# Kernel tuning notes

Measured on AMD Instinct MI355X. Metric: run time of the kernel, lower is better.

Reference implementation:

```python
import jax, jax.numpy as jnp
import numpy as np

N = 50000       # nodes
E = 800000      # directed edges (before self-loops)
F_IN = 256      # input node features
HID = 64        # hidden_channels
HEADS = 4       # heads of conv1
NEG_SLOPE = 0.2 # PyG GATConv LeakyReLU slope


def setup_inputs() -> dict:
    key = jax.random.key(0)
    ks = jax.random.split(key, 10)
    x = jax.random.normal(ks[0], (N, F_IN), dtype=jnp.float32)
    edge_index = jax.random.randint(ks[1], (2, E), 0, N, dtype=jnp.int32)
    # GATConv params: lin weight [F_in, H*C], att_src/att_dst [H, C], bias
    W1 = jax.random.normal(ks[2], (F_IN, HEADS * HID), jnp.float32) * (1.0 / np.sqrt(F_IN))
    att_src1 = jax.random.normal(ks[3], (HEADS, HID), jnp.float32) * (1.0 / np.sqrt(HID))
    att_dst1 = jax.random.normal(ks[4], (HEADS, HID), jnp.float32) * (1.0 / np.sqrt(HID))
    b1 = jnp.zeros((HEADS * HID,), jnp.float32)
    W2 = jax.random.normal(ks[5], (HEADS * HID, HID), jnp.float32) * (1.0 / np.sqrt(HEADS * HID))
    att_src2 = jax.random.normal(ks[6], (1, HID), jnp.float32) * (1.0 / np.sqrt(HID))
    att_dst2 = jax.random.normal(ks[7], (1, HID), jnp.float32) * (1.0 / np.sqrt(HID))
    b2 = jnp.zeros((HID,), jnp.float32)
    return dict(x=x, edge_index=edge_index, W1=W1, att_src1=att_src1,
                att_dst1=att_dst1, b1=b1, W2=W2, att_src2=att_src2,
                att_dst2=att_dst2, b2=b2)


def gat_layer(x, src, dst, W, a_src, a_dst, bias, heads, ch, concat):
    n = x.shape[0]
    xh = (x @ W).reshape(n, heads, ch)                      # [N,H,C]
    al_s = jnp.einsum('nhc,hc->nh', xh, a_src)              # [N,H]
    al_d = jnp.einsum('nhc,hc->nh', xh, a_dst)
    e = jax.nn.leaky_relu(al_s[src] + al_d[dst], NEG_SLOPE) # [Etot,H]
    # segment softmax over incoming edges of each dst node
    m = jax.ops.segment_max(e, dst, num_segments=n)         # every node has a self-loop
    ex = jnp.exp(e - m[dst])
    den = jax.ops.segment_sum(ex, dst, num_segments=n)
    alpha = ex / (den[dst] + 1e-16)                         # [Etot,H]
    out = jax.ops.segment_sum(alpha[:, :, None] * xh[src], dst, num_segments=n)  # [N,H,C]
    out = out.reshape(n, heads * ch) if concat else out.mean(axis=1)
    return out + bias


def reference(x, edge_index, W1, att_src1, att_dst1, b1, W2, att_src2, att_dst2, b2):
    # GATConv default add_self_loops=True
    loops = jnp.arange(x.shape[0], dtype=edge_index.dtype)
    src = jnp.concatenate([edge_index[0], loops])
    dst = jnp.concatenate([edge_index[1], loops])
    h = jax.nn.elu(gat_layer(x, src, dst, W1, att_src1, att_dst1, b1, HEADS, HID, True))
    # dropout omitted (eval mode)
    out = jax.nn.elu(gat_layer(h, src, dst, W2, att_src2, att_dst2, b2, 1, HID, False))
    return out
```

## Files before the change

kernel.cpp:

```cpp
#include <hip/hip_runtime.h>
#include <math.h>


using short8_t  = __attribute__((ext_vector_type(8))) short;
using f32x4     = __attribute__((ext_vector_type(4))) float;
using ushort4v  = __attribute__((ext_vector_type(4))) unsigned short;
using ushort8v  = __attribute__((ext_vector_type(8))) unsigned short;
using half4     = __attribute__((ext_vector_type(4))) _Float16;

__device__ __forceinline__ float leaky02(float t) { return t > 0.f ? t : 0.2f * t; }
__device__ __forceinline__ float elu1(float t) { return t > 0.f ? t : (__expf(t) - 1.f); }

__device__ __forceinline__ unsigned short bf16_rne(float f) {
  unsigned u = __float_as_uint(f);
  unsigned r = u + 0x7FFFu + ((u >> 16) & 1u);
  return (unsigned short)(r >> 16);
}
__device__ __forceinline__ float bf16_to_f(unsigned short h) {
  return __uint_as_float(((unsigned)h) << 16);
}


__global__ __launch_bounds__(256) void count_kernel(const int* __restrict__ dst,
                                                    int* __restrict__ count, int E) {
  int e = blockIdx.x * blockDim.x + threadIdx.x;
  if (e < E) atomicAdd(&count[dst[e]], 1);
}

__global__ __launch_bounds__(256) void scan1_kernel(const int* __restrict__ count,
                                                    int* __restrict__ locpre,
                                                    int* __restrict__ bsum, int n) {
  __shared__ int sh[256];
  int t = threadIdx.x;
  int node = blockIdx.x * 256 + t;
  int v = (node < n) ? (1 + count[node]) : 0;
  sh[t] = v;
  __syncthreads();
  for (int off = 1; off < 256; off <<= 1) {
    int u = (t >= off) ? sh[t - off] : 0;
    __syncthreads();
    sh[t] += u;
    __syncthreads();
  }
  if (node < n) locpre[node] = sh[t] - v;
  if (t == 255) bsum[blockIdx.x] = sh[255];
}

__global__ __launch_bounds__(256) void scan2_kernel(int* __restrict__ bsum, int nb) {
  __shared__ int sh[256];
  int t = threadIdx.x;
  int v = (t < nb) ? bsum[t] : 0;
  sh[t] = v;
  __syncthreads();
  for (int off = 1; off < 256; off <<= 1) {
    int u = (t >= off) ? sh[t - off] : 0;
    __syncthreads();
    sh[t] += u;
    __syncthreads();
  }
  if (t < nb) bsum[t] = sh[t] - v;
}

__global__ __launch_bounds__(256) void scan3_kernel(const int* __restrict__ locpre,
                                                    const int* __restrict__ bsum,
                                                    int* __restrict__ offsets,
                                                    int* __restrict__ csr,
                                                    int* __restrict__ cursor,
                                                    int n, int Etot) {
  int node = blockIdx.x * 256 + threadIdx.x;
  if (node >= n) return;
  int o = bsum[blockIdx.x] + locpre[node];
  offsets[node] = o;
  csr[o] = node;
  cursor[node] = 0;
  if (node == n - 1) offsets[n] = Etot;
}

__global__ __launch_bounds__(256) void scatter_kernel(const int* __restrict__ src,
                                                      const int* __restrict__ dst,
                                                      const int* __restrict__ offsets,
                                                      int* __restrict__ cursor,
                                                      int* __restrict__ csr, int E) {
  int e = blockIdx.x * blockDim.x + threadIdx.x;
  if (e < E) {
    int d = dst[e];
    int pos = atomicAdd(&cursor[d], 1);
    csr[offsets[d] + 1 + pos] = src[e];
  }
}

__global__ __launch_bounds__(256) void convB_kernel(const float* __restrict__ W,
                                                    unsigned short* __restrict__ Bth,
                                                    unsigned short* __restrict__ Btl, int N) {
  int idx = blockIdx.x * blockDim.x + threadIdx.x;
  if (idx >= N * 64) return;
  int n = idx >> 6;
  int k4 = (idx & 63) * 4;
  ushort4v hi, lo;
#pragma unroll
  for (int i = 0; i < 4; ++i) {
    float w = W[(size_t)(k4 + i) * N + n];
    hi[i] = bf16_rne(w);
    lo[i] = bf16_rne(w - bf16_to_f(hi[i]));
  }
  size_t base = (size_t)n * 256 + k4;
  *(ushort4v*)&Bth[base] = hi;
  *(ushort4v*)&Btl[base] = lo;
}

template <int BN, int WR, int WC, int H, bool AF32>
__global__ __launch_bounds__(256) void gemm_fused(
    const float* __restrict__ Af,
    const unsigned short* __restrict__ Ah, const unsigned short* __restrict__ Al,
    const unsigned short* __restrict__ Bh, const unsigned short* __restrict__ Bl,
    const float* __restrict__ asrc, const float* __restrict__ adst,
    _Float16* __restrict__ xh, float* __restrict__ als, float* __restrict__ ald,
    int M, int N) {
  constexpr int BM = 128, BK = 32, KTOT = 256;
  constexpr int WM = BM / WR, WN = BN / WC;
  constexpr int MR = WM / 16, NR = WN / 16;
  constexpr int BROUNDS = (BN * 4) / 256;
  __shared__ __align__(16) unsigned short lsAh[BM * BK];
  __shared__ __align__(16) unsigned short lsAl[BM * BK];
  __shared__ __align__(16) unsigned short lsBh[BN * BK];
  __shared__ __align__(16) unsigned short lsBl[BN * BK];
  const int tid = threadIdx.x;
  const int lane = tid & 63;
  const int w = tid >> 6;
  const int wr = w / WC, wc = w % WC;
  const int bm = blockIdx.x * BM;
  const int bn = blockIdx.y * BN;

  f32x4 acc[MR][NR];
#pragma unroll
  for (int i = 0; i < MR; ++i)
#pragma unroll
    for (int j = 0; j < NR; ++j) acc[i][j] = (f32x4){0.f, 0.f, 0.f, 0.f};

  for (int k0 = 0; k0 < KTOT; k0 += BK) {
#pragma unroll
    for (int rnd = 0; rnd < 2; ++rnd) {
      int id = rnd * 256 + tid;
      int row = id >> 2, c0 = id & 3;
      int cs = c0 ^ ((row >> 1) & 3);
      bool ok = (bm + row) < M;
      ushort8v hi, lo;
      if (AF32) {
        float vv[8];
        if (ok) {
          float4 v0 = *(const float4*)&Af[(size_t)(bm + row) * 256 + k0 + c0 * 8];
          float4 v1 = *(const float4*)&Af[(size_t)(bm + row) * 256 + k0 + c0 * 8 + 4];
          vv[0] = v0.x; vv[1] = v0.y; vv[2] = v0.z; vv[3] = v0.w;
          vv[4] = v1.x; vv[5] = v1.y; vv[6] = v1.z; vv[7] = v1.w;
        } else {
#pragma unroll
          for (int i = 0; i < 8; ++i) vv[i] = 0.f;
        }
#pragma unroll
        for (int i = 0; i < 8; ++i) {
          hi[i] = bf16_rne(vv[i]);
          lo[i] = bf16_rne(vv[i] - bf16_to_f(hi[i]));
        }
      } else {
        if (ok) {
          hi = *(const ushort8v*)&Ah[(size_t)(bm + row) * 256 + k0 + c0 * 8];
          lo = *(const ushort8v*)&Al[(size_t)(bm + row) * 256 + k0 + c0 * 8];
        } else {
#pragma unroll
          for (int i = 0; i < 8; ++i) { hi[i] = 0; lo[i] = 0; }
        }
      }
      *(ushort8v*)&lsAh[row * BK + cs * 8] = hi;
      *(ushort8v*)&lsAl[row * BK + cs * 8] = lo;
    }
#pragma unroll
    for (int rnd = 0; rnd < BROUNDS; ++rnd) {
      int id = rnd * 256 + tid;
      int row = id >> 2, c0 = id & 3;
      int cs = c0 ^ ((row >> 1) & 3);
      *(ushort8v*)&lsBh[row * BK + cs * 8] =
          *(const ushort8v*)&Bh[(size_t)(bn + row) * 256 + k0 + c0 * 8];
      *(ushort8v*)&lsBl[row * BK + cs * 8] =
          *(const ushort8v*)&Bl[(size_t)(bn + row) * 256 + k0 + c0 * 8];
    }
    __syncthreads();
    short8_t afh[MR], afl[MR], bfh[NR], bfl[NR];
#pragma unroll
    for (int mr = 0; mr < MR; ++mr) {
      int rr = wr * WM + mr * 16 + (lane & 15);
      int kc = (lane >> 4) ^ ((rr >> 1) & 3);
      afh[mr] = *(const short8_t*)&lsAh[rr * BK + kc * 8];
      afl[mr] = *(const short8_t*)&lsAl[rr * BK + kc * 8];
    }
#pragma unroll
    for (int nr = 0; nr < NR; ++nr) {
      int rn = wc * WN + nr * 16 + (lane & 15);
      int kc = (lane >> 4) ^ ((rn >> 1) & 3);
      bfh[nr] = *(const short8_t*)&lsBh[rn * BK + kc * 8];
      bfl[nr] = *(const short8_t*)&lsBl[rn * BK + kc * 8];
    }
#pragma unroll
    for (int mr = 0; mr < MR; ++mr)
#pragma unroll
      for (int nr = 0; nr < NR; ++nr) {
        acc[mr][nr] = __builtin_amdgcn_mfma_f32_16x16x32_bf16(afh[mr], bfh[nr], acc[mr][nr], 0, 0, 0);
        acc[mr][nr] = __builtin_amdgcn_mfma_f32_16x16x32_bf16(afl[mr], bfh[nr], acc[mr][nr], 0, 0, 0);
        acc[mr][nr] = __builtin_amdgcn_mfma_f32_16x16x32_bf16(afh[mr], bfl[nr], acc[mr][nr], 0, 0, 0);
      }
    __syncthreads();
  }

  float as_[NR], ad_[NR];
#pragma unroll
  for (int nr = 0; nr < NR; ++nr) {
    int c = bn + wc * WN + nr * 16 + (lane & 15);
    as_[nr] = asrc[c];
    ad_[nr] = adst[c];
  }
  const int head = (bn + wc * WN) >> 6;
#pragma unroll
  for (int mr = 0; mr < MR; ++mr) {
#pragma unroll
    for (int j = 0; j < 4; ++j) {
      int r = bm + wr * WM + mr * 16 + (lane >> 4) * 4 + j;
      bool ok = r < M;
      float s = 0.f, d = 0.f;
#pragma unroll
      for (int nr = 0; nr < NR; ++nr) {
        float v = acc[mr][nr][j];
        if (ok) {
          int c = bn + wc * WN + nr * 16 + (lane & 15);
          xh[(size_t)r * N + c] = (_Float16)v;
        }
        s += v * as_[nr];
        d += v * ad_[nr];
      }
#pragma unroll
      for (int m = 1; m <= 8; m <<= 1) {
        s += __shfl_xor(s, m);
        d += __shfl_xor(d, m);
      }
      if (ok && (lane & 15) == 0) {
        als[r * H + head] = s;
        ald[r * H + head] = d;
      }
    }
  }
}

__global__ __launch_bounds__(256) void agg1_kernel(const _Float16* __restrict__ xh,
                                                   const float* __restrict__ als,
                                                   const float* __restrict__ ald,
                                                   const int* __restrict__ offsets,
                                                   const int* __restrict__ csr,
                                                   const float* __restrict__ bias,
                                                   unsigned short* __restrict__ A2h,
                                                   unsigned short* __restrict__ A2l, int n) {
  int node = (blockIdx.x * blockDim.x + threadIdx.x) >> 6;
  int lane = threadIdx.x & 63;
  if (node >= n) return;
  int h = lane >> 4;
  int beg = offsets[node], end = offsets[node + 1];
  float ad = ald[node * 4 + h];
  float den = 0.f;
  float ax = 0.f, ay = 0.f, az = 0.f, aw = 0.f;
  int e = beg;
  for (; e + 4 <= end; e += 4) {
    int s0 = csr[e], s1 = csr[e + 1], s2 = csr[e + 2], s3 = csr[e + 3];
    float a0 = als[s0 * 4 + h], a1 = als[s1 * 4 + h];
    float a2 = als[s2 * 4 + h], a3 = als[s3 * 4 + h];
    half4 x0 = *(const half4*)&xh[(size_t)s0 * 256 + 4 * lane];
    half4 x1 = *(const half4*)&xh[(size_t)s1 * 256 + 4 * lane];
    half4 x2 = *(const half4*)&xh[(size_t)s2 * 256 + 4 * lane];
    half4 x3 = *(const half4*)&xh[(size_t)s3 * 256 + 4 * lane];
    float e0 = __expf(leaky02(a0 + ad));
    float e1 = __expf(leaky02(a1 + ad));
    float e2 = __expf(leaky02(a2 + ad));
    float e3 = __expf(leaky02(a3 + ad));
    den += (e0 + e1) + (e2 + e3);
    ax += e0 * (float)x0[0] + e1 * (float)x1[0] + e2 * (float)x2[0] + e3 * (float)x3[0];
    ay += e0 * (float)x0[1] + e1 * (float)x1[1] + e2 * (float)x2[1] + e3 * (float)x3[1];
    az += e0 * (float)x0[2] + e1 * (float)x1[2] + e2 * (float)x2[2] + e3 * (float)x3[2];
    aw += e0 * (float)x0[3] + e1 * (float)x1[3] + e2 * (float)x2[3] + e3 * (float)x3[3];
  }
  for (; e < end; ++e) {
    int s = csr[e];
    float a = als[s * 4 + h];
    half4 xv = *(const half4*)&xh[(size_t)s * 256 + 4 * lane];
    float ex = __expf(leaky02(a + ad));
    den += ex;
    ax += ex * (float)xv[0]; ay += ex * (float)xv[1];
    az += ex * (float)xv[2]; aw += ex * (float)xv[3];
  }
  float inv = 1.f / (den + 1e-16f);
  float4 b = *(const float4*)&bias[4 * lane];
  float o0 = elu1(ax * inv + b.x);
  float o1 = elu1(ay * inv + b.y);
  float o2 = elu1(az * inv + b.z);
  float o3 = elu1(aw * inv + b.w);
  ushort4v hi, lo;
  hi[0] = bf16_rne(o0); lo[0] = bf16_rne(o0 - bf16_to_f(hi[0]));
  hi[1] = bf16_rne(o1); lo[1] = bf16_rne(o1 - bf16_to_f(hi[1]));
  hi[2] = bf16_rne(o2); lo[2] = bf16_rne(o2 - bf16_to_f(hi[2]));
  hi[3] = bf16_rne(o3); lo[3] = bf16_rne(o3 - bf16_to_f(hi[3]));
  size_t base = (size_t)node * 256 + 4 * lane;
  *(ushort4v*)&A2h[base] = hi;
  *(ushort4v*)&A2l[base] = lo;
}

__global__ __launch_bounds__(256) void agg2_kernel(const _Float16* __restrict__ xh,
                                                   const float* __restrict__ als,
                                                   const float* __restrict__ ald,
                                                   const int* __restrict__ offsets,
                                                   const int* __restrict__ csr,
                                                   const float* __restrict__ bias,
                                                   float* __restrict__ out, int n) {
  int node = (blockIdx.x * blockDim.x + threadIdx.x) >> 6;
  int lane = threadIdx.x & 63;
  if (node >= n) return;
  int g = lane >> 4, li = lane & 15;
  int beg = offsets[node], end = offsets[node + 1];
  float ad = ald[node];
  float den = 0.f;
  float ax = 0.f, ay = 0.f, az = 0.f, aw = 0.f;
  for (int e0 = beg; e0 < end; e0 += 4) {
    int e = e0 + g;
    if (e < end) {
      int s = csr[e];
      float ex = __expf(leaky02(als[s] + ad));
      half4 xv = *(const half4*)&xh[(size_t)s * 64 + 4 * li];
      den += ex;
      ax += ex * (float)xv[0]; ay += ex * (float)xv[1];
      az += ex * (float)xv[2]; aw += ex * (float)xv[3];
    }
  }
#pragma unroll
  for (int m = 16; m <= 32; m <<= 1) {
    den += __shfl_xor(den, m);
    ax += __shfl_xor(ax, m);
    ay += __shfl_xor(ay, m);
    az += __shfl_xor(az, m);
    aw += __shfl_xor(aw, m);
  }
  if (g == 0) {
    float inv = 1.f / (den + 1e-16f);
    float4 b = *(const float4*)&bias[4 * li];
    float4 o;
    o.x = elu1(ax * inv + b.x);
    o.y = elu1(ay * inv + b.y);
    o.z = elu1(az * inv + b.z);
    o.w = elu1(aw * inv + b.w);
    *(float4*)&out[(size_t)node * 64 + 4 * li] = o;
  }
}


extern "C" void kernel_launch(void* const* d_in, const int* in_sizes, int n_in,
                              void* d_out, int out_size, void* d_ws, size_t ws_size,
                              hipStream_t stream) {
  const float* x   = (const float*)d_in[0];
  const int*   ei  = (const int*)d_in[1];
  const float* W1  = (const float*)d_in[2];
  const float* as1 = (const float*)d_in[3];
  const float* ad1 = (const float*)d_in[4];
  const float* b1  = (const float*)d_in[5];
  const float* W2  = (const float*)d_in[6];
  const float* as2 = (const float*)d_in[7];
  const float* ad2 = (const float*)d_in[8];
  const float* b2  = (const float*)d_in[9];
  float* out = (float*)d_out;

  const int E = in_sizes[1] / 2;
  const int n = in_sizes[0] / 256;
  const int Mpad = ((n + 127) / 128) * 128;
  const int nb = (n + 255) / 256;

  size_t off = 0;
  auto alloc = [&](size_t bytes) -> void* {
    void* p = (char*)d_ws + off;
    off += (bytes + 511) & ~(size_t)511;
    return p;
  };
  _Float16* xh = (_Float16*)alloc((size_t)n * 256 * 2);
  unsigned short* A2h = (unsigned short*)alloc((size_t)Mpad * 256 * 2);
  unsigned short* A2l = (unsigned short*)alloc((size_t)Mpad * 256 * 2);
  unsigned short* Bh1 = (unsigned short*)alloc((size_t)256 * 256 * 2);
  unsigned short* Bl1 = (unsigned short*)alloc((size_t)256 * 256 * 2);
  unsigned short* Bh2 = (unsigned short*)alloc((size_t)64 * 256 * 2);
  unsigned short* Bl2 = (unsigned short*)alloc((size_t)64 * 256 * 2);
  float* als1v = (float*)alloc((size_t)n * 4 * 4);
  float* ald1v = (float*)alloc((size_t)n * 4 * 4);
  float* als2v = (float*)alloc((size_t)n * 4);
  float* ald2v = (float*)alloc((size_t)n * 4);
  int* count   = (int*)alloc((size_t)n * 4);
  int* cursor  = (int*)alloc((size_t)n * 4);
  int* offsets = (int*)alloc((size_t)(n + 1) * 4);
  int* locpre  = (int*)alloc((size_t)n * 4);
  int* bsum    = (int*)alloc(256 * 4);
  int* csr     = (int*)alloc((size_t)(E + n) * 4);

  const int* srcv = ei;
  const int* dstv = ei + E;

  hipMemsetAsync(count, 0, (size_t)n * 4, stream);
  count_kernel<<<(E + 255) / 256, 256, 0, stream>>>(dstv, count, E);
  scan1_kernel<<<nb, 256, 0, stream>>>(count, locpre, bsum, n);
  scan2_kernel<<<1, 256, 0, stream>>>(bsum, nb);
  scan3_kernel<<<nb, 256, 0, stream>>>(locpre, bsum, offsets, csr, cursor, n, E + n);
  scatter_kernel<<<(E + 255) / 256, 256, 0, stream>>>(srcv, dstv, offsets, cursor, csr, E);

  convB_kernel<<<(256 * 64 + 255) / 256, 256, 0, stream>>>(W1, Bh1, Bl1, 256);
  convB_kernel<<<(64 * 64 + 255) / 256, 256, 0, stream>>>(W2, Bh2, Bl2, 64);

  gemm_fused<128, 2, 2, 4, true><<<dim3(Mpad / 128, 2), 256, 0, stream>>>(
      x, nullptr, nullptr, Bh1, Bl1, as1, ad1, xh, als1v, ald1v, n, 256);
  agg1_kernel<<<(n + 3) / 4, 256, 0, stream>>>(xh, als1v, ald1v, offsets, csr, b1, A2h, A2l, n);

  gemm_fused<64, 4, 1, 1, false><<<dim3(Mpad / 128, 1), 256, 0, stream>>>(
      nullptr, A2h, A2l, Bh2, Bl2, as2, ad2, xh, als2v, ald2v, n, 64);
  agg2_kernel<<<(n + 3) / 4, 256, 0, stream>>>(xh, als2v, ald2v, offsets, csr, b2, out, n);
}
```

Baseline: 354.9 us.

## Pad CSR rows to multiples of four, use fp16 layer-2 GEMM, single-pass layer-1 GEMM

Each node's CSR segment is now padded to a multiple of four with a sentinel node whose attention logit is -1e30. This lets the aggregation kernels use vectorized int4 index loads with no tail loops or bounds checks. Layer 2 now uses a single fp16 MFMA GEMM in place of the three-pass split-bf16 scheme, and agg1 writes fp16 activations, which halves intermediate storage. The layer-1 GEMM becomes one 512-thread block covering all 256 output columns, so each A tile is loaded and converted only once. The cost is extra padded CSR entries and lower precision in layer 2.

Measured after the change: 338.8 us. 4.5% less time.

```diff
diff --git a/kernel.cpp b/kernel.cpp
--- a/kernel.cpp
+++ b/kernel.cpp
@@ -3,6 +3,7 @@
 
 
 using short8_t  = __attribute__((ext_vector_type(8))) short;
+using half8_t   = __attribute__((ext_vector_type(8))) _Float16;
 using f32x4     = __attribute__((ext_vector_type(4))) float;
 using ushort4v  = __attribute__((ext_vector_type(4))) unsigned short;
 using ushort8v  = __attribute__((ext_vector_type(8))) unsigned short;
@@ -33,7 +34,7 @@
   __shared__ int sh[256];
   int t = threadIdx.x;
   int node = blockIdx.x * 256 + t;
-  int v = (node < n) ? (1 + count[node]) : 0;
+  int v = (node < n) ? ((count[node] + 4) & ~3) : 0;
   sh[t] = v;
   __syncthreads();
   for (int off = 1; off < 256; off <<= 1) {
@@ -61,19 +62,29 @@
   if (t < nb) bsum[t] = sh[t] - v;
 }
 
-__global__ __launch_bounds__(256) void scan3_kernel(const int* __restrict__ locpre,
+__global__ __launch_bounds__(256) void scan3_kernel(const int* __restrict__ count,
+                                                    const int* __restrict__ locpre,
                                                     const int* __restrict__ bsum,
                                                     int* __restrict__ offsets,
                                                     int* __restrict__ csr,
                                                     int* __restrict__ cursor,
-                                                    int n, int Etot) {
+                                                    float* __restrict__ als1s,
+                                                    float* __restrict__ als2s,
+                                                    int n) {
   int node = blockIdx.x * 256 + threadIdx.x;
   if (node >= n) return;
   int o = bsum[blockIdx.x] + locpre[node];
+  int cnt = count[node];
+  int padlen = (cnt + 4) & ~3;
   offsets[node] = o;
   csr[o] = node;
+  for (int p = 1 + cnt; p < padlen; ++p) csr[o + p] = n;
   cursor[node] = 0;
-  if (node == n - 1) offsets[n] = Etot;
+  if (node == n - 1) offsets[n] = o + padlen;
+  if (node == 0) {
+    als1s[0] = -1e30f; als1s[1] = -1e30f; als1s[2] = -1e30f; als1s[3] = -1e30f;
+    als2s[0] = -1e30f;
+  }
 }
 
 __global__ __launch_bounds__(256) void scatter_kernel(const int* __restrict__ src,
@@ -108,28 +119,146 @@
   *(ushort4v*)&Btl[base] = lo;
 }
 
-template <int BN, int WR, int WC, int H, bool AF32>
-__global__ __launch_bounds__(256) void gemm_fused(
+__global__ __launch_bounds__(256) void convB2_kernel(const float* __restrict__ W,
+                                                     _Float16* __restrict__ Bt, int N) {
+  int idx = blockIdx.x * blockDim.x + threadIdx.x;
+  if (idx >= N * 64) return;
+  int n = idx >> 6;
+  int k4 = (idx & 63) * 4;
+  half4 v;
+#pragma unroll
+  for (int i = 0; i < 4; ++i) v[i] = (_Float16)W[(size_t)(k4 + i) * N + n];
+  *(half4*)&Bt[(size_t)n * 256 + k4] = v;
+}
+
+__global__ __launch_bounds__(512) void gemm1_fused(
     const float* __restrict__ Af,
-    const unsigned short* __restrict__ Ah, const unsigned short* __restrict__ Al,
     const unsigned short* __restrict__ Bh, const unsigned short* __restrict__ Bl,
     const float* __restrict__ asrc, const float* __restrict__ adst,
-    _Float16* __restrict__ xh, float* __restrict__ als, float* __restrict__ ald,
-    int M, int N) {
-  constexpr int BM = 128, BK = 32, KTOT = 256;
-  constexpr int WM = BM / WR, WN = BN / WC;
-  constexpr int MR = WM / 16, NR = WN / 16;
-  constexpr int BROUNDS = (BN * 4) / 256;
+    _Float16* __restrict__ xh, float* __restrict__ als, float* __restrict__ ald, int M) {
+  constexpr int BM = 128, BK = 32, KTOT = 256, NW = 256;
+  constexpr int MR = 4, NR = 4;
   __shared__ __align__(16) unsigned short lsAh[BM * BK];
   __shared__ __align__(16) unsigned short lsAl[BM * BK];
-  __shared__ __align__(16) unsigned short lsBh[BN * BK];
-  __shared__ __align__(16) unsigned short lsBl[BN * BK];
+  __shared__ __align__(16) unsigned short lsBh[NW * BK];
+  __shared__ __align__(16) unsigned short lsBl[NW * BK];
   const int tid = threadIdx.x;
   const int lane = tid & 63;
   const int w = tid >> 6;
-  const int wr = w / WC, wc = w % WC;
+  const int wr = w >> 2, wc = w & 3;
   const int bm = blockIdx.x * BM;
-  const int bn = blockIdx.y * BN;
+
+  f32x4 acc[MR][NR];
+#pragma unroll
+  for (int i = 0; i < MR; ++i)
+#pragma unroll
+    for (int j = 0; j < NR; ++j) acc[i][j] = (f32x4){0.f, 0.f, 0.f, 0.f};
+
+  for (int k0 = 0; k0 < KTOT; k0 += BK) {
+    {
+      int row = tid >> 2, c0 = tid & 3;
+      int cs = c0 ^ ((row >> 1) & 3);
+      float vv[8];
+      if (bm + row < M) {
+        float4 v0 = *(const float4*)&Af[(size_t)(bm + row) * 256 + k0 + c0 * 8];
+        float4 v1 = *(const float4*)&Af[(size_t)(bm + row) * 256 + k0 + c0 * 8 + 4];
+        vv[0] = v0.x; vv[1] = v0.y; vv[2] = v0.z; vv[3] = v0.w;
+        vv[4] = v1.x; vv[5] = v1.y; vv[6] = v1.z; vv[7] = v1.w;
+      } else {
+#pragma unroll
+        for (int i = 0; i < 8; ++i) vv[i] = 0.f;
+      }
+      ushort8v hi, lo;
+#pragma unroll
+      for (int i = 0; i < 8; ++i) {
+        hi[i] = bf16_rne(vv[i]);
+        lo[i] = bf16_rne(vv[i] - bf16_to_f(hi[i]));
+      }
+      *(ushort8v*)&lsAh[row * BK + cs * 8] = hi;
+      *(ushort8v*)&lsAl[row * BK + cs * 8] = lo;
+    }
+#pragma unroll
+    for (int rnd = 0; rnd < 2; ++rnd) {
+      int id = rnd * 512 + tid;
+      int row = id >> 2, c0 = id & 3;
+      int cs = c0 ^ ((row >> 1) & 3);
+      *(ushort8v*)&lsBh[row * BK + cs * 8] =
+          *(const ushort8v*)&Bh[(size_t)row * 256 + k0 + c0 * 8];
+      *(ushort8v*)&lsBl[row * BK + cs * 8] =
+          *(const ushort8v*)&Bl[(size_t)row * 256 + k0 + c0 * 8];
+    }
+    __syncthreads();
+    short8_t afh[MR], afl[MR];
+#pragma unroll
+    for (int mr = 0; mr < MR; ++mr) {
+      int rr = wr * 64 + mr * 16 + (lane & 15);
+      int kc = (lane >> 4) ^ ((rr >> 1) & 3);
+      afh[mr] = *(const short8_t*)&lsAh[rr * BK + kc * 8];
+      afl[mr] = *(const short8_t*)&lsAl[rr * BK + kc * 8];
+    }
+#pragma unroll
+    for (int nr = 0; nr < NR; ++nr) {
+      int rn = wc * 64 + nr * 16 + (lane & 15);
+      int kc = (lane >> 4) ^ ((rn >> 1) & 3);
+      short8_t bh = *(const short8_t*)&lsBh[rn * BK + kc * 8];
+      short8_t bl = *(const short8_t*)&lsBl[rn * BK + kc * 8];
+#pragma unroll
+      for (int mr = 0; mr < MR; ++mr) {
+        acc[mr][nr] = __builtin_amdgcn_mfma_f32_16x16x32_bf16(afh[mr], bh, acc[mr][nr], 0, 0, 0);
+        acc[mr][nr] = __builtin_amdgcn_mfma_f32_16x16x32_bf16(afl[mr], bh, acc[mr][nr], 0, 0, 0);
+        acc[mr][nr] = __builtin_amdgcn_mfma_f32_16x16x32_bf16(afh[mr], bl, acc[mr][nr], 0, 0, 0);
+      }
+    }
+    __syncthreads();
+  }
+
+  float as_[NR], ad_[NR];
+#pragma unroll
+  for (int nr = 0; nr < NR; ++nr) {
+    int c = wc * 64 + nr * 16 + (lane & 15);
+    as_[nr] = asrc[c];
+    ad_[nr] = adst[c];
+  }
+#pragma unroll
+  for (int mr = 0; mr < MR; ++mr) {
+#pragma unroll
+    for (int j = 0; j < 4; ++j) {
+      int r = bm + wr * 64 + mr * 16 + (lane >> 4) * 4 + j;
+      bool ok = r < M;
+      float s = 0.f, d = 0.f;
+#pragma unroll
+      for (int nr = 0; nr < NR; ++nr) {
+        float v = acc[mr][nr][j];
+        if (ok) xh[(size_t)r * 256 + wc * 64 + nr * 16 + (lane & 15)] = (_Float16)v;
+        s += v * as_[nr];
+        d += v * ad_[nr];
+      }
+#pragma unroll
+      for (int m = 1; m <= 8; m <<= 1) {
+        s += __shfl_xor(s, m);
+        d += __shfl_xor(d, m);
+      }
+      if (ok && (lane & 15) == 0) {
+        als[r * 4 + wc] = s;
+        ald[r * 4 + wc] = d;
+      }
+    }
+  }
+}
+
+__global__ __launch_bounds__(256) void gemm2_fused(
+    const _Float16* __restrict__ A,
+    const _Float16* __restrict__ Bt,
+    const float* __restrict__ asrc, const float* __restrict__ adst,
+    _Float16* __restrict__ xh, float* __restrict__ als, float* __restrict__ ald, int M) {
+  constexpr int BM = 128, BK = 32, KTOT = 256, NW = 64;
+  constexpr int MR = 2, NR = 4;
+  __shared__ __align__(16) _Float16 lsA[BM * BK];
+  __shared__ __align__(16) _Float16 lsB[NW * BK];
+  const int tid = threadIdx.x;
+  const int lane = tid & 63;
+  const int wr = tid >> 6;
+  const int bm = blockIdx.x * BM;
 
   f32x4 acc[MR][NR];
 #pragma unroll
@@ -143,95 +272,55 @@
       int id = rnd * 256 + tid;
       int row = id >> 2, c0 = id & 3;
       int cs = c0 ^ ((row >> 1) & 3);
-      bool ok = (bm + row) < M;
-      ushort8v hi, lo;
-      if (AF32) {
-        float vv[8];
-        if (ok) {
-          float4 v0 = *(const float4*)&Af[(size_t)(bm + row) * 256 + k0 + c0 * 8];
-          float4 v1 = *(const float4*)&Af[(size_t)(bm + row) * 256 + k0 + c0 * 8 + 4];
-          vv[0] = v0.x; vv[1] = v0.y; vv[2] = v0.z; vv[3] = v0.w;
-          vv[4] = v1.x; vv[5] = v1.y; vv[6] = v1.z; vv[7] = v1.w;
-        } else {
-#pragma unroll
-          for (int i = 0; i < 8; ++i) vv[i] = 0.f;
-        }
-#pragma unroll
-        for (int i = 0; i < 8; ++i) {
-          hi[i] = bf16_rne(vv[i]);
-          lo[i] = bf16_rne(vv[i] - bf16_to_f(hi[i]));
-        }
-      } else {
-        if (ok) {
-          hi = *(const ushort8v*)&Ah[(size_t)(bm + row) * 256 + k0 + c0 * 8];
-          lo = *(const ushort8v*)&Al[(size_t)(bm + row) * 256 + k0 + c0 * 8];
-        } else {
-#pragma unroll
-          for (int i = 0; i < 8; ++i) { hi[i] = 0; lo[i] = 0; }
-        }
-      }
-      *(ushort8v*)&lsAh[row * BK + cs * 8] = hi;
-      *(ushort8v*)&lsAl[row * BK + cs * 8] = lo;
-    }
-#pragma unroll
-    for (int rnd = 0; rnd < BROUNDS; ++rnd) {
-      int id = rnd * 256 + tid;
-      int row = id >> 2, c0 = id & 3;
+      *(half8_t*)&lsA[row * BK + cs * 8] =
+          *(const half8_t*)&A[(size_t)(bm + row) * 256 + k0 + c0 * 8];
+    }
+    {
+      int row = tid >> 2, c0 = tid & 3;
       int cs = c0 ^ ((row >> 1) & 3);
-      *(ushort8v*)&lsBh[row * BK + cs * 8] =
-          *(const ushort8v*)&Bh[(size_t)(bn + row) * 256 + k0 + c0 * 8];
-      *(ushort8v*)&lsBl[row * BK + cs * 8] =
-          *(const ushort8v*)&Bl[(size_t)(bn + row) * 256 + k0 + c0 * 8];
-    }
-    __syncthreads();
-    short8_t afh[MR], afl[MR], bfh[NR], bfl[NR];
+      *(half8_t*)&lsB[row * BK + cs * 8] =
+          *(const half8_t*)&Bt[(size_t)row * 256 + k0 + c0 * 8];
+    }
+    __syncthreads();
+    half8_t af[MR], bf[NR];
 #pragma unroll
     for (int mr = 0; mr < MR; ++mr) {
-      int rr = wr * WM + mr * 16 + (lane & 15);
+      int rr = wr * 32 + mr * 16 + (lane & 15);
       int kc = (lane >> 4) ^ ((rr >> 1) & 3);
-      afh[mr] = *(const short8_t*)&lsAh[rr * BK + kc * 8];
-      afl[mr] = *(const short8_t*)&lsAl[rr * BK + kc * 8];
+      af[mr] = *(const half8_t*)&lsA[rr * BK + kc * 8];
     }
 #pragma unroll
     for (int nr = 0; nr < NR; ++nr) {
-      int rn = wc * WN + nr * 16 + (lane & 15);
+      int rn = nr * 16 + (lane & 15);
       int kc = (lane >> 4) ^ ((rn >> 1) & 3);
-      bfh[nr] = *(const short8_t*)&lsBh[rn * BK + kc * 8];
-      bfl[nr] = *(const short8_t*)&lsBl[rn * BK + kc * 8];
-    }
+      bf[nr] = *(const half8_t*)&lsB[rn * BK + kc * 8];
+    }
+    __syncthreads();
 #pragma unroll
     for (int mr = 0; mr < MR; ++mr)
 #pragma unroll
-      for (int nr = 0; nr < NR; ++nr) {
-        acc[mr][nr] = __builtin_amdgcn_mfma_f32_16x16x32_bf16(afh[mr], bfh[nr], acc[mr][nr], 0, 0, 0);
-        acc[mr][nr] = __builtin_amdgcn_mfma_f32_16x16x32_bf16(afl[mr], bfh[nr], acc[mr][nr], 0, 0, 0);
-        acc[mr][nr] = __builtin_amdgcn_mfma_f32_16x16x32_bf16(afh[mr], bfl[nr], acc[mr][nr], 0, 0, 0);
-      }
-    __syncthreads();
+      for (int nr = 0; nr < NR; ++nr)
+        acc[mr][nr] = __builtin_amdgcn_mfma_f32_16x16x32_f16(af[mr], bf[nr], acc[mr][nr], 0, 0, 0);
   }
 
   float as_[NR], ad_[NR];
 #pragma unroll
   for (int nr = 0; nr < NR; ++nr) {
-    int c = bn + wc * WN + nr * 16 + (lane & 15);
+    int c = nr * 16 + (lane & 15);
     as_[nr] = asrc[c];
     ad_[nr] = adst[c];
   }
-  const int head = (bn + wc * WN) >> 6;
 #pragma unroll
   for (int mr = 0; mr < MR; ++mr) {
 #pragma unroll
     for (int j = 0; j < 4; ++j) {
-      int r = bm + wr * WM + mr * 16 + (lane >> 4) * 4 + j;
+      int r = bm + wr * 32 + mr * 16 + (lane >> 4) * 4 + j;
       bool ok = r < M;
       float s = 0.f, d = 0.f;
 #pragma unroll
       for (int nr = 0; nr < NR; ++nr) {
         float v = acc[mr][nr][j];
-        if (ok) {
-          int c = bn + wc * WN + nr * 16 + (lane & 15);
-          xh[(size_t)r * N + c] = (_Float16)v;
-        }
+        if (ok) xh[(size_t)r * 64 + nr * 16 + (lane & 15)] = (_Float16)v;
         s += v * as_[nr];
         d += v * ad_[nr];
       }
@@ -241,8 +330,8 @@
         d += __shfl_xor(d, m);
       }
       if (ok && (lane & 15) == 0) {
-        als[r * H + head] = s;
-        ald[r * H + head] = d;
+        als[r] = s;
+        ald[r] = d;
       }
     }
   }
@@ -254,8 +343,7 @@
                                                    const int* __restrict__ offsets,
                                                    const int* __restrict__ csr,
                                                    const float* __restrict__ bias,
-                                                   unsigned short* __restrict__ A2h,
-                                                   unsigned short* __restrict__ A2l, int n) {
+                                                   _Float16* __restrict__ A2, int n) {
   int node = (blockIdx.x * blockDim.x + threadIdx.x) >> 6;
   int lane = threadIdx.x & 63;
   if (node >= n) return;
@@ -264,15 +352,14 @@
   float ad = ald[node * 4 + h];
   float den = 0.f;
   float ax = 0.f, ay = 0.f, az = 0.f, aw = 0.f;
-  int e = beg;
-  for (; e + 4 <= end; e += 4) {
-    int s0 = csr[e], s1 = csr[e + 1], s2 = csr[e + 2], s3 = csr[e + 3];
-    float a0 = als[s0 * 4 + h], a1 = als[s1 * 4 + h];
-    float a2 = als[s2 * 4 + h], a3 = als[s3 * 4 + h];
-    half4 x0 = *(const half4*)&xh[(size_t)s0 * 256 + 4 * lane];
-    half4 x1 = *(const half4*)&xh[(size_t)s1 * 256 + 4 * lane];
-    half4 x2 = *(const half4*)&xh[(size_t)s2 * 256 + 4 * lane];
-    half4 x3 = *(const half4*)&xh[(size_t)s3 * 256 + 4 * lane];
+  for (int e = beg; e < end; e += 4) {
+    int4 s4 = *(const int4*)&csr[e];
+    float a0 = als[s4.x * 4 + h], a1 = als[s4.y * 4 + h];
+    float a2 = als[s4.z * 4 + h], a3 = als[s4.w * 4 + h];
+    half4 x0 = *(const half4*)&xh[(size_t)s4.x * 256 + 4 * lane];
+    half4 x1 = *(const half4*)&xh[(size_t)s4.y * 256 + 4 * lane];
+    half4 x2 = *(const half4*)&xh[(size_t)s4.z * 256 + 4 * lane];
+    half4 x3 = *(const half4*)&xh[(size_t)s4.w * 256 + 4 * lane];
     float e0 = __expf(leaky02(a0 + ad));
     float e1 = __expf(leaky02(a1 + ad));
     float e2 = __expf(leaky02(a2 + ad));
@@ -283,29 +370,14 @@
     az += e0 * (float)x0[2] + e1 * (float)x1[2] + e2 * (float)x2[2] + e3 * (float)x3[2];
     aw += e0 * (float)x0[3] + e1 * (float)x1[3] + e2 * (float)x2[3] + e3 * (float)x3[3];
   }
-  for (; e < end; ++e) {
-    int s = csr[e];
-    float a = als[s * 4 + h];
-    half4 xv = *(const half4*)&xh[(size_t)s * 256 + 4 * lane];
-    float ex = __expf(leaky02(a + ad));
-    den += ex;
-    ax += ex * (float)xv[0]; ay += ex * (float)xv[1];
-    az += ex * (float)xv[2]; aw += ex * (float)xv[3];
-  }
   float inv = 1.f / (den + 1e-16f);
   float4 b = *(const float4*)&bias[4 * lane];
-  float o0 = elu1(ax * inv + b.x);
-  float o1 = elu1(ay * inv + b.y);
-  float o2 = elu1(az * inv + b.z);
-  float o3 = elu1(aw * inv + b.w);
-  ushort4v hi, lo;
-  hi[0] = bf16_rne(o0); lo[0] = bf16_rne(o0 - bf16_to_f(hi[0]));
-  hi[1] = bf16_rne(o1); lo[1] = bf16_rne(o1 - bf16_to_f(hi[1]));
-  hi[2] = bf16_rne(o2); lo[2] = bf16_rne(o2 - bf16_to_f(hi[2]));
-  hi[3] = bf16_rne(o3); lo[3] = bf16_rne(o3 - bf16_to_f(hi[3]));
-  size_t base = (size_t)node * 256 + 4 * lane;
-  *(ushort4v*)&A2h[base] = hi;
-  *(ushort4v*)&A2l[base] = lo;
+  half4 o;
+  o[0] = (_Float16)elu1(ax * inv + b.x);
+  o[1] = (_Float16)elu1(ay * inv + b.y);
+  o[2] = (_Float16)elu1(az * inv + b.z);
+  o[3] = (_Float16)elu1(aw * inv + b.w);
+  *(half4*)&A2[(size_t)node * 256 + 4 * lane] = o;
 }
 
 __global__ __launch_bounds__(256) void agg2_kernel(const _Float16* __restrict__ xh,
@@ -324,15 +396,12 @@
   float den = 0.f;
   float ax = 0.f, ay = 0.f, az = 0.f, aw = 0.f;
   for (int e0 = beg; e0 < end; e0 += 4) {
-    int e = e0 + g;
-    if (e < end) {
-      int s = csr[e];
-      float ex = __expf(leaky02(als[s] + ad));
-      half4 xv = *(const half4*)&xh[(size_t)s * 64 + 4 * li];
-      den += ex;
-      ax += ex * (float)xv[0]; ay += ex * (float)xv[1];
-      az += ex * (float)xv[2]; aw += ex * (float)xv[3];
-    }
+    int s = csr[e0 + g];
+    float ex = __expf(leaky02(als[s] + ad));
+    half4 xv = *(const half4*)&xh[(size_t)s * 64 + 4 * li];
+    den += ex;
+    ax += ex * (float)xv[0]; ay += ex * (float)xv[1];
+    az += ex * (float)xv[2]; aw += ex * (float)xv[3];
   }
 #pragma unroll
   for (int m = 16; m <= 32; m <<= 1) {
@@ -381,23 +450,21 @@
     off += (bytes + 511) & ~(size_t)511;
     return p;
   };
-  _Float16* xh = (_Float16*)alloc((size_t)n * 256 * 2);
-  unsigned short* A2h = (unsigned short*)alloc((size_t)Mpad * 256 * 2);
-  unsigned short* A2l = (unsigned short*)alloc((size_t)Mpad * 256 * 2);
+  _Float16* xh  = (_Float16*)alloc((size_t)(n + 1) * 256 * 2);
+  _Float16* A2  = (_Float16*)alloc((size_t)Mpad * 256 * 2);
   unsigned short* Bh1 = (unsigned short*)alloc((size_t)256 * 256 * 2);
   unsigned short* Bl1 = (unsigned short*)alloc((size_t)256 * 256 * 2);
-  unsigned short* Bh2 = (unsigned short*)alloc((size_t)64 * 256 * 2);
-  unsigned short* Bl2 = (unsigned short*)alloc((size_t)64 * 256 * 2);
-  float* als1v = (float*)alloc((size_t)n * 4 * 4);
+  _Float16* Bt2 = (_Float16*)alloc((size_t)64 * 256 * 2);
+  float* als1v = (float*)alloc((size_t)(n + 1) * 4 * 4);
   float* ald1v = (float*)alloc((size_t)n * 4 * 4);
-  float* als2v = (float*)alloc((size_t)n * 4);
+  float* als2v = (float*)alloc((size_t)(n + 1) * 4);
   float* ald2v = (float*)alloc((size_t)n * 4);
   int* count   = (int*)alloc((size_t)n * 4);
   int* cursor  = (int*)alloc((size_t)n * 4);
   int* offsets = (int*)alloc((size_t)(n + 1) * 4);
   int* locpre  = (int*)alloc((size_t)n * 4);
   int* bsum    = (int*)alloc(256 * 4);
-  int* csr     = (int*)alloc((size_t)(E + n) * 4);
+  int* csr     = (int*)alloc((size_t)(E + 4 * n) * 4);
 
   const int* srcv = ei;
   const int* dstv = ei + E;
@@ -406,17 +473,16 @@
   count_kernel<<<(E + 255) / 256, 256, 0, stream>>>(dstv, count, E);
   scan1_kernel<<<nb, 256, 0, stream>>>(count, locpre, bsum, n);
   scan2_kernel<<<1, 256, 0, stream>>>(bsum, nb);
-  scan3_kernel<<<nb, 256, 0, stream>>>(locpre, bsum, offsets, csr, cursor, n, E + n);
+  scan3_kernel<<<nb, 256, 0, stream>>>(count, locpre, bsum, offsets, csr, cursor,
+                                       als1v + (size_t)n * 4, als2v + n, n);
   scatter_kernel<<<(E + 255) / 256, 256, 0, stream>>>(srcv, dstv, offsets, cursor, csr, E);
 
   convB_kernel<<<(256 * 64 + 255) / 256, 256, 0, stream>>>(W1, Bh1, Bl1, 256);
-  convB_kernel<<<(64 * 64 + 255) / 256, 256, 0, stream>>>(W2, Bh2, Bl2, 64);
-
-  gemm_fused<128, 2, 2, 4, true><<<dim3(Mpad / 128, 2), 256, 0, stream>>>(
-      x, nullptr, nullptr, Bh1, Bl1, as1, ad1, xh, als1v, ald1v, n, 256);
-  agg1_kernel<<<(n + 3) / 4, 256, 0, stream>>>(xh, als1v, ald1v, offsets, csr, b1, A2h, A2l, n);
-
-  gemm_fused<64, 4, 1, 1, false><<<dim3(Mpad / 128, 1), 256, 0, stream>>>(
-      nullptr, A2h, A2l, Bh2, Bl2, as2, ad2, xh, als2v, ald2v, n, 64);
+  convB2_kernel<<<(64 * 64 + 255) / 256, 256, 0, stream>>>(W2, Bt2, 64);
+
+  gemm1_fused<<<Mpad / 128, 512, 0, stream>>>(x, Bh1, Bl1, as1, ad1, xh, als1v, ald1v, n);
+  agg1_kernel<<<(n + 3) / 4, 256, 0, stream>>>(xh, als1v, ald1v, offsets, csr, b1, A2, n);
+
+  gemm2_fused<<<Mpad / 128, 256, 0, stream>>>(A2, Bt2, as2, ad2, xh, als2v, ald2v, n);
   agg2_kernel<<<(n + 3) / 4, 256, 0, stream>>>(xh, als2v, ald2v, offsets, csr, b2, out, n);
 }
```
